# Optimization experiments

Hardware: AMD Instinct MI355X
Metric: run time of the kernel (lower is better)

The kernel has to match this reference:

```python
import jax, jax.numpy as jnp
import numpy as np
import math

B, C, H, W = 8, 256, 64, 64
CQK = C // 8

def _conv1x1(x, w, b):
    # x: [B,C,H,W], w: [O,C], b: [O]  (1x1 conv == per-pixel linear)
    return jnp.einsum('bchw,oc->bohw', x, w) + b[None, :, None, None]

def setup_inputs() -> dict:
    key = jax.random.key(0)
    ks = jax.random.split(key, 7)
    inputs = jax.random.normal(ks[0], (B, C, H, W), dtype=jnp.float32)
    # init_weight: normal(0, sqrt(2/(k*k*out_channels))) for 1x1 convs
    wq = jax.random.normal(ks[1], (CQK, C), dtype=jnp.float32) * math.sqrt(2.0 / CQK)
    wk = jax.random.normal(ks[2], (CQK, C), dtype=jnp.float32) * math.sqrt(2.0 / CQK)
    wv = jax.random.normal(ks[3], (C, C), dtype=jnp.float32) * math.sqrt(2.0 / C)
    bq = jnp.zeros((CQK,), dtype=jnp.float32)
    bk = jnp.zeros((CQK,), dtype=jnp.float32)
    bv = jnp.zeros((C,), dtype=jnp.float32)
    # torch init is zeros(1); use nonzero so the attention path contributes
    alpha = jnp.full((1,), 0.5, dtype=jnp.float32)
    return {"inputs": inputs, "wq": wq, "bq": bq, "wk": wk, "bk": bk,
            "wv": wv, "bv": bv, "alpha": alpha}

def reference(inputs, wq, bq, wk, bk, wv, bv, alpha):
    b, c, h, w = inputs.shape
    n = h * w
    q = _conv1x1(inputs, wq, bq).reshape(b, -1, n)          # [B, C/8, N]
    k = _conv1x1(inputs, wk, bk).reshape(b, -1, n)          # [B, C/8, N]
    v = _conv1x1(inputs, wv, bv).reshape(b, c, n)           # [B, C, N]
    # attention_weight[b, i, j] = q[:, i] . k[:, j]
    attn = jnp.einsum('bdi,bdj->bij', q, k)                 # [B, N, N]
    attn = jax.nn.softmax(attn, axis=-1)
    # value @ attn^T : out[b, c, i] = sum_j v[b, c, j] * attn[b, i, j]
    out = jnp.einsum('bcj,bij->bci', v, attn)               # [B, C, N]
    return alpha[0] * out.reshape(inputs.shape) + inputs
```

## Files before the change

### kernel.cpp

```cpp
#include <hip/hip_runtime.h>
#include <math.h>

#define B_  8
#define C_  256
#define N_  4096
#define NJC (N_ / 128)
#define PLD 136
#define LOG2E 1.4426950408889634f

using frag  = __attribute__((ext_vector_type(8))) short;
using f32x4 = __attribute__((ext_vector_type(4))) float;

__device__ __forceinline__ unsigned short f2bf(float f) {
    unsigned u = __float_as_uint(f);
    u += 0x7fffu + ((u >> 16) & 1u);
    return (unsigned short)(u >> 16);
}
__device__ __forceinline__ float bf2f(unsigned short h) {
    return __uint_as_float(((unsigned)h) << 16);
}
#define PK2(a, b) (((unsigned)(a)) | (((unsigned)(b)) << 16))

__device__ __forceinline__ f32x4 fmax4(f32x4 a, f32x4 b) {
    f32x4 r;
    r[0] = fmaxf(a[0], b[0]); r[1] = fmaxf(a[1], b[1]);
    r[2] = fmaxf(a[2], b[2]); r[3] = fmaxf(a[3], b[3]);
    return r;
}

__device__ __forceinline__ float exp2_raw(float x) {
    float r;
    asm("v_exp_f32 %0, %1" : "=v"(r) : "v"(x));
    return r;
}

__global__ __launch_bounds__(256) void wprep_kernel(
    const float* __restrict__ wq, const float* __restrict__ wk,
    const float* __restrict__ wv,
    unsigned short* __restrict__ whf, unsigned short* __restrict__ wlf)
{
    const int fid  = blockIdx.x * 256 + threadIdx.x;
    if (fid >= 20 * 8 * 64) return;
    const int g    = fid >> 9;
    const int kc   = (fid >> 6) & 7;
    const int lane = fid & 63;
    const int r16  = lane & 15, q = lane >> 4;

    const float* src; int row;
    if (g < 2)      { src = wq; row = g * 16 + r16; }
    else if (g < 4) { src = wk; row = (g - 2) * 16 + r16; }
    else            { src = wv; row = (g - 4) * 16 + r16; }

    const float scl = (g < 2) ? LOG2E : 1.0f;
    const float* wp = src + row * 256 + kc * 32 + q * 8;
    float v[8];
#pragma unroll
    for (int j = 0; j < 8; ++j) v[j] = wp[j] * scl;

    unsigned short h[8];
#pragma unroll
    for (int j = 0; j < 8; ++j) h[j] = f2bf(v[j]);
    uint4 U;
    U.x = PK2(h[0], h[1]); U.y = PK2(h[2], h[3]);
    U.z = PK2(h[4], h[5]); U.w = PK2(h[6], h[7]);
    *(uint4*)&whf[(size_t)fid * 8] = U;

    if (g < 4) {
        unsigned short l[8];
#pragma unroll
        for (int j = 0; j < 8; ++j) l[j] = f2bf(v[j] - bf2f(h[j]));
        uint4 V;
        V.x = PK2(l[0], l[1]); V.y = PK2(l[2], l[3]);
        V.z = PK2(l[4], l[5]); V.w = PK2(l[6], l[7]);
        *(uint4*)&wlf[(size_t)fid * 8] = V;
    }
}

__global__ __launch_bounds__(256, 4) void proj_kernel(
    const float* __restrict__ x,
    const float* __restrict__ bq, const float* __restrict__ bk,
    const float* __restrict__ bv,
    const unsigned short* __restrict__ whf, const unsigned short* __restrict__ wlf,
    unsigned short* __restrict__ qh, unsigned short* __restrict__ ql,
    unsigned short* __restrict__ kh, unsigned short* __restrict__ kl,
    unsigned short* __restrict__ vbf)
{
    __shared__ unsigned xpk[32 * 260 + 4];

    const int tid  = threadIdx.x;
    const int w    = tid >> 6;
    const int lane = tid & 63;
    const int quad = lane >> 4;
    const int l16  = lane & 15;
    const int n0   = blockIdx.x * 32;
    const int b    = blockIdx.y;

    {
        const int p  = tid & 31;
        const int cb = tid >> 5;
        const float* xbase = x + (size_t)b * C_ * N_ + n0 + p;
#pragma unroll 16
        for (int s = 0; s < 32; ++s) {
            const int c = s * 8 + cb;
            const float v = xbase[(size_t)c * N_];
            const unsigned short hb = f2bf(v);
            const unsigned short lb = f2bf(v - bf2f(hb));
            xpk[p * 260 + c] = (((unsigned)hb) << 16) | lb;
        }
    }
    __syncthreads();

    const frag* wh = (const frag*)whf;
    const frag* wl = (const frag*)wlf;

    f32x4 aqk[2];
    f32x4 av[4][2];
#pragma unroll
    for (int ps = 0; ps < 2; ++ps) {
        aqk[ps] = (f32x4){0.f, 0.f, 0.f, 0.f};
#pragma unroll
        for (int vg = 0; vg < 4; ++vg) av[vg][ps] = (f32x4){0.f, 0.f, 0.f, 0.f};
    }

    for (int kc = 0; kc < 8; ++kc) {
        const frag ah = wh[(w * 8 + kc) * 64 + lane];
        const frag al = wl[(w * 8 + kc) * 64 + lane];
        frag avw[4];
#pragma unroll
        for (int vg = 0; vg < 4; ++vg)
            avw[vg] = wh[((4 + w * 4 + vg) * 8 + kc) * 64 + lane];

#pragma unroll
        for (int ps = 0; ps < 2; ++ps) {
            const unsigned* row = &xpk[(ps * 16 + l16) * 260 + kc * 32 + quad * 8];
            const uint4 A  = *(const uint4*)row;
            const uint4 Bv = *(const uint4*)(row + 4);
            frag bh, bl;
            unsigned* bhp = (unsigned*)&bh;
            unsigned* blp = (unsigned*)&bl;
            bhp[0] = __builtin_amdgcn_perm(A.y,  A.x,  0x07060302u);
            bhp[1] = __builtin_amdgcn_perm(A.w,  A.z,  0x07060302u);
            bhp[2] = __builtin_amdgcn_perm(Bv.y, Bv.x, 0x07060302u);
            bhp[3] = __builtin_amdgcn_perm(Bv.w, Bv.z, 0x07060302u);
            blp[0] = __builtin_amdgcn_perm(A.y,  A.x,  0x05040100u);
            blp[1] = __builtin_amdgcn_perm(A.w,  A.z,  0x05040100u);
            blp[2] = __builtin_amdgcn_perm(Bv.y, Bv.x, 0x05040100u);
            blp[3] = __builtin_amdgcn_perm(Bv.w, Bv.z, 0x05040100u);

            aqk[ps] = __builtin_amdgcn_mfma_f32_16x16x32_bf16(ah, bh, aqk[ps], 0, 0, 0);
            aqk[ps] = __builtin_amdgcn_mfma_f32_16x16x32_bf16(al, bh, aqk[ps], 0, 0, 0);
            aqk[ps] = __builtin_amdgcn_mfma_f32_16x16x32_bf16(ah, bl, aqk[ps], 0, 0, 0);
#pragma unroll
            for (int vg = 0; vg < 4; ++vg)
                av[vg][ps] = __builtin_amdgcn_mfma_f32_16x16x32_bf16(
                    avw[vg], bh, av[vg][ps], 0, 0, 0);
        }
    }

    {
        const bool isq = (w < 2);
        const float* bias = isq ? bq : bk;
        const float bscl = isq ? LOG2E : 1.0f;
        const int dbase = (isq ? w : w - 2) * 16 + quad * 4;
        unsigned short* dsth = isq ? qh : kh;
        unsigned short* dstl = isq ? ql : kl;
        float bvals[4];
#pragma unroll
        for (int r = 0; r < 4; ++r) bvals[r] = bias[dbase + r] * bscl;
#pragma unroll
        for (int ps = 0; ps < 2; ++ps) {
            const int n = n0 + ps * 16 + l16;
            unsigned short hs[4], ls[4];
#pragma unroll
            for (int r = 0; r < 4; ++r) {
                const float f = aqk[ps][r] + bvals[r];
                hs[r] = f2bf(f);
                ls[r] = f2bf(f - bf2f(hs[r]));
            }
            const size_t off = ((size_t)(b * N_ + n)) * 32 + dbase;
            *(uint2*)&dsth[off] = make_uint2(PK2(hs[0], hs[1]), PK2(hs[2], hs[3]));
            *(uint2*)&dstl[off] = make_uint2(PK2(ls[0], ls[1]), PK2(ls[2], ls[3]));
        }
    }
#pragma unroll
    for (int vg = 0; vg < 4; ++vg)
#pragma unroll
        for (int ps = 0; ps < 2; ++ps) {
            const int n = n0 + ps * 16 + l16;
#pragma unroll
            for (int r = 0; r < 4; ++r) {
                const int c = (w * 4 + vg) * 16 + quad * 4 + r;
                vbf[((size_t)b * C_ + c) * N_ + n] = f2bf(av[vg][ps][r] + bv[c]);
            }
        }
}

__global__ __launch_bounds__(512, 2) void attn_kernel(
    const unsigned short* __restrict__ qh, const unsigned short* __restrict__ ql,
    const unsigned short* __restrict__ khg, const unsigned short* __restrict__ klg,
    const unsigned short* __restrict__ vbf,
    const float* __restrict__ x, const float* __restrict__ alpha_p,
    float* __restrict__ out)
{
    __shared__ __align__(16) short kbuf[2][2][128 * 32];
    __shared__ __align__(16) short p_s[2][128 * PLD];
    __shared__ __align__(16) float alpha_s[2][128];
    __shared__ __align__(16) float l_s[128];

    const int tid  = threadIdx.x;
    const int w    = tid >> 6;
    const int lane = tid & 63;
    const int quad = lane >> 4;
    const int l16  = lane & 15;
    const int bid  = blockIdx.x;
    const int b    = bid & 7;
    const int i0   = (bid >> 3) * 128;
    const int wi   = w >> 2;
    const int wc   = w & 3;

    const size_t qoff = ((size_t)(b * N_ + i0 + w * 16 + l16)) * 32 + quad * 8;
    const frag qhf = *(const frag*)(qh + qoff);
    const frag qlf = *(const frag*)(ql + qoff);

    const unsigned short* khb = khg + (size_t)b * N_ * 32;
    const unsigned short* klb = klg + (size_t)b * N_ * 32;
    const unsigned short* vb  = vbf + (size_t)b * C_ * N_;

    f32x4 o[4][4];
#pragma unroll
    for (int it = 0; it < 4; ++it)
#pragma unroll
        for (int ct = 0; ct < 4; ++ct)
            o[it][ct] = (f32x4){0.f, 0.f, 0.f, 0.f};

    float m_run = -INFINITY, l_run = 0.f;

    const int r_st  = w * 16 + l16;
    const int qc_st = quad;
    const int gsto  = r_st * 32 + qc_st * 8;
    const int lsto  = qc_st * 1024 + r_st * 8;

    frag vf[4][4];

    {
        const uint4 h0 = *(const uint4*)(khb + gsto);
        const uint4 l0 = *(const uint4*)(klb + gsto);
        *(uint4*)&kbuf[0][0][lsto] = h0;
        *(uint4*)&kbuf[0][1][lsto] = l0;
    }
    __syncthreads();

    for (int jc = 0; jc < NJC; ++jc) {
        const int bf = jc & 1;

        f32x4 st[8];
#pragma unroll
        for (int js = 0; js < 8; ++js) {
            const frag ka  = *(const frag*)&kbuf[bf][0][quad * 1024 + (js * 16 + l16) * 8];
            const frag kb2 = *(const frag*)&kbuf[bf][1][quad * 1024 + (js * 16 + l16) * 8];
            f32x4 s = (f32x4){0.f, 0.f, 0.f, 0.f};
            s = __builtin_amdgcn_mfma_f32_16x16x32_bf16(ka, qhf, s, 0, 0, 0);
            s = __builtin_amdgcn_mfma_f32_16x16x32_bf16(ka, qlf, s, 0, 0, 0);
            s = __builtin_amdgcn_mfma_f32_16x16x32_bf16(kb2, qhf, s, 0, 0, 0);
            st[js] = s;
        }

        const int jn = (jc + 1 < NJC) ? jc + 1 : jc;
        const uint4 knh = *(const uint4*)(khb + (size_t)jn * 4096 + gsto);
        const uint4 knl = *(const uint4*)(klb + (size_t)jn * 4096 + gsto);

        if (jc > 0) {
#pragma unroll
            for (int it = 0; it < 4; ++it) {
                const f32x4 alf = *(const f32x4*)&alpha_s[bf ^ 1][wi * 64 + it * 16 + quad * 4];
#pragma unroll
                for (int r = 0; r < 4; ++r) {
#pragma unroll
                    for (int ct = 0; ct < 4; ++ct) o[it][ct][r] *= alf[r];
                }
            }
#pragma unroll
            for (int ks = 0; ks < 4; ++ks) {
#pragma unroll
                for (int it = 0; it < 4; ++it) {
                    const frag pf = *(const frag*)&p_s[bf ^ 1][(wi * 64 + it * 16 + l16) * PLD
                                                              + ks * 32 + quad * 8];
#pragma unroll
                    for (int ct = 0; ct < 4; ++ct)
                        o[it][ct] = __builtin_amdgcn_mfma_f32_16x16x32_bf16(
                            pf, vf[ks][ct], o[it][ct], 0, 0, 0);
                }
            }
        }

#pragma unroll
        for (int ks = 0; ks < 4; ++ks)
#pragma unroll
            for (int ct = 0; ct < 4; ++ct)
                vf[ks][ct] = *(const frag*)(vb
                    + (size_t)(wc * 64 + ct * 16 + l16) * N_
                    + jc * 128 + ks * 32 + quad * 8);

        f32x4 t0 = fmax4(fmax4(st[0], st[1]), fmax4(st[2], st[3]));
        f32x4 t1 = fmax4(fmax4(st[4], st[5]), fmax4(st[6], st[7]));
        t0 = fmax4(t0, t1);
        float mx = fmaxf(fmaxf(t0[0], t0[1]), fmaxf(t0[2], t0[3]));
        mx = fmaxf(mx, __shfl_xor(mx, 16));
        mx = fmaxf(mx, __shfl_xor(mx, 32));
        const float mnew = fmaxf(m_run, mx);
        const float sc   = exp2_raw(m_run - mnew);

        f32x4 ps4 = (f32x4){0.f, 0.f, 0.f, 0.f};
#pragma unroll
        for (int js = 0; js < 8; ++js) {
#pragma unroll
            for (int r = 0; r < 4; ++r) st[js][r] = exp2_raw(st[js][r] - mnew);
            ps4[0] += st[js][0]; ps4[1] += st[js][1];
            ps4[2] += st[js][2]; ps4[3] += st[js][3];
        }
        float ps = (ps4[0] + ps4[1]) + (ps4[2] + ps4[3]);
        ps += __shfl_xor(ps, 16);
        ps += __shfl_xor(ps, 32);
        l_run = l_run * sc + ps;
        m_run = mnew;
        if (quad == 0) alpha_s[bf][w * 16 + l16] = sc;

#pragma unroll
        for (int js = 0; js < 8; ++js) {
            const unsigned a0 = __float_as_uint(st[js][0]) + 0x8000u;
            const unsigned a1 = __float_as_uint(st[js][1]) + 0x8000u;
            const unsigned a2 = __float_as_uint(st[js][2]) + 0x8000u;
            const unsigned a3 = __float_as_uint(st[js][3]) + 0x8000u;
            const unsigned p01 = __builtin_amdgcn_perm(a1, a0, 0x07060302u);
            const unsigned p23 = __builtin_amdgcn_perm(a3, a2, 0x07060302u);
            *(uint2*)&p_s[bf][(w * 16 + l16) * PLD + js * 16 + quad * 4] =
                make_uint2(p01, p23);
        }

        *(uint4*)&kbuf[bf ^ 1][0][lsto] = knh;
        *(uint4*)&kbuf[bf ^ 1][1][lsto] = knl;

        __syncthreads();
    }

    {
        const int bl = (NJC - 1) & 1;
#pragma unroll
        for (int it = 0; it < 4; ++it) {
            const f32x4 alf = *(const f32x4*)&alpha_s[bl][wi * 64 + it * 16 + quad * 4];
#pragma unroll
            for (int r = 0; r < 4; ++r) {
#pragma unroll
                for (int ct = 0; ct < 4; ++ct) o[it][ct][r] *= alf[r];
            }
        }
#pragma unroll
        for (int ks = 0; ks < 4; ++ks) {
#pragma unroll
            for (int it = 0; it < 4; ++it) {
                const frag pf = *(const frag*)&p_s[bl][(wi * 64 + it * 16 + l16) * PLD
                                                       + ks * 32 + quad * 8];
#pragma unroll
                for (int ct = 0; ct < 4; ++ct)
                    o[it][ct] = __builtin_amdgcn_mfma_f32_16x16x32_bf16(
                        pf, vf[ks][ct], o[it][ct], 0, 0, 0);
            }
        }
    }

    if (quad == 0) l_s[w * 16 + l16] = l_run;
    __syncthreads();
    const float av = alpha_p[0];

#pragma unroll
    for (int it = 0; it < 4; ++it) {
        const f32x4 lv = *(const f32x4*)&l_s[wi * 64 + it * 16 + quad * 4];
        float invl[4];
#pragma unroll
        for (int r = 0; r < 4; ++r) invl[r] = 1.f / lv[r];
#pragma unroll
        for (int ct = 0; ct < 4; ++ct) {
            const int c = wc * 64 + ct * 16 + l16;
            const size_t base = (size_t)b * C_ * N_ + (size_t)c * N_
                                + i0 + wi * 64 + it * 16 + quad * 4;
            const float4 xv = *(const float4*)(x + base);
            float4 ov;
            ov.x = av * (o[it][ct][0] * invl[0]) + xv.x;
            ov.y = av * (o[it][ct][1] * invl[1]) + xv.y;
            ov.z = av * (o[it][ct][2] * invl[2]) + xv.z;
            ov.w = av * (o[it][ct][3] * invl[3]) + xv.w;
            *(float4*)(out + base) = ov;
        }
    }
}

extern "C" void kernel_launch(void* const* d_in, const int* in_sizes, int n_in,
                              void* d_out, int out_size, void* d_ws, size_t ws_size,
                              hipStream_t stream)
{
    const float* x  = (const float*)d_in[0];
    const float* wq = (const float*)d_in[1];
    const float* bq = (const float*)d_in[2];
    const float* wk = (const float*)d_in[3];
    const float* bk = (const float*)d_in[4];
    const float* wv = (const float*)d_in[5];
    const float* bv = (const float*)d_in[6];
    const float* al = (const float*)d_in[7];
    float* out = (float*)d_out;

    char* ws = (char*)d_ws;
    unsigned short* qh  = (unsigned short*)(ws + 0);
    unsigned short* ql  = (unsigned short*)(ws + (size_t)2  * 1024 * 1024);
    unsigned short* kh  = (unsigned short*)(ws + (size_t)4  * 1024 * 1024);
    unsigned short* kl  = (unsigned short*)(ws + (size_t)6  * 1024 * 1024);
    unsigned short* vbf = (unsigned short*)(ws + (size_t)8  * 1024 * 1024);
    unsigned short* whf = (unsigned short*)(ws + (size_t)24 * 1024 * 1024);
    unsigned short* wlf = (unsigned short*)(ws + (size_t)24 * 1024 * 1024 + 256 * 1024);

    wprep_kernel<<<40, 256, 0, stream>>>(wq, wk, wv, whf, wlf);
    proj_kernel<<<dim3(N_ / 32, B_), 256, 0, stream>>>(
        x, bq, bk, bv, whf, wlf, qh, ql, kh, kl, vbf);
    attn_kernel<<<dim3(256), 512, 0, stream>>>(
        qh, ql, kh, kl, vbf, x, al, out);
}
```

Before: 252.0 us.

## Warp-specialize attention kernel into score/softmax and PV producer-consumer groups

Splits the 8 waves into two roles. Four waves compute QK scores and the online softmax for 32 rows each and write P to shared memory. The other four waves consume P from the previous chunk and accumulate the PV product over all 128 rows for their 64 channels. This aims to overlap the exp/softmax work with the MFMA-heavy PV stage through a one-chunk software pipeline. In exchange, each consumer wave holds twice as many accumulators (8x4 f32x4), which raises register pressure, and the producer waves sit idle during the epilogue.

```diff
diff --git a/kernel.cpp b/kernel.cpp
--- a/kernel.cpp
+++ b/kernel.cpp
@@ -215,32 +215,37 @@
     const int bid  = blockIdx.x;
     const int b    = bid & 7;
     const int i0   = (bid >> 3) * 128;
-    const int wi   = w >> 2;
-    const int wc   = w & 3;
-
-    const size_t qoff = ((size_t)(b * N_ + i0 + w * 16 + l16)) * 32 + quad * 8;
-    const frag qhf = *(const frag*)(qh + qoff);
-    const frag qlf = *(const frag*)(ql + qoff);
+    const bool isS = (w < 4);
+    const int  w2  = w & 3;
 
     const unsigned short* khb = khg + (size_t)b * N_ * 32;
     const unsigned short* klb = klg + (size_t)b * N_ * 32;
     const unsigned short* vb  = vbf + (size_t)b * C_ * N_;
 
-    f32x4 o[4][4];
-#pragma unroll
-    for (int it = 0; it < 4; ++it)
+    frag qhf[2], qlf[2];
+    if (isS) {
+#pragma unroll
+        for (int s2 = 0; s2 < 2; ++s2) {
+            const size_t qoff = ((size_t)(b * N_ + i0 + w2 * 32 + s2 * 16 + l16)) * 32
+                                + quad * 8;
+            qhf[s2] = *(const frag*)(qh + qoff);
+            qlf[s2] = *(const frag*)(ql + qoff);
+        }
+    }
+    float m_run[2] = {-INFINITY, -INFINITY};
+    float l_run[2] = {0.f, 0.f};
+
+    f32x4 o[8][4];
+#pragma unroll
+    for (int it = 0; it < 8; ++it)
 #pragma unroll
         for (int ct = 0; ct < 4; ++ct)
             o[it][ct] = (f32x4){0.f, 0.f, 0.f, 0.f};
-
-    float m_run = -INFINITY, l_run = 0.f;
 
     const int r_st  = w * 16 + l16;
     const int qc_st = quad;
     const int gsto  = r_st * 32 + qc_st * 8;
     const int lsto  = qc_st * 1024 + r_st * 8;
-
-    frag vf[4][4];
 
     {
         const uint4 h0 = *(const uint4*)(khb + gsto);
@@ -250,146 +255,146 @@
     }
     __syncthreads();
 
-    for (int jc = 0; jc < NJC; ++jc) {
-        const int bf = jc & 1;
-
-        f32x4 st[8];
-#pragma unroll
-        for (int js = 0; js < 8; ++js) {
-            const frag ka  = *(const frag*)&kbuf[bf][0][quad * 1024 + (js * 16 + l16) * 8];
-            const frag kb2 = *(const frag*)&kbuf[bf][1][quad * 1024 + (js * 16 + l16) * 8];
-            f32x4 s = (f32x4){0.f, 0.f, 0.f, 0.f};
-            s = __builtin_amdgcn_mfma_f32_16x16x32_bf16(ka, qhf, s, 0, 0, 0);
-            s = __builtin_amdgcn_mfma_f32_16x16x32_bf16(ka, qlf, s, 0, 0, 0);
-            s = __builtin_amdgcn_mfma_f32_16x16x32_bf16(kb2, qhf, s, 0, 0, 0);
-            st[js] = s;
-        }
-
-        const int jn = (jc + 1 < NJC) ? jc + 1 : jc;
-        const uint4 knh = *(const uint4*)(khb + (size_t)jn * 4096 + gsto);
-        const uint4 knl = *(const uint4*)(klb + (size_t)jn * 4096 + gsto);
-
-        if (jc > 0) {
-#pragma unroll
-            for (int it = 0; it < 4; ++it) {
-                const f32x4 alf = *(const f32x4*)&alpha_s[bf ^ 1][wi * 64 + it * 16 + quad * 4];
-#pragma unroll
-                for (int r = 0; r < 4; ++r) {
-#pragma unroll
-                    for (int ct = 0; ct < 4; ++ct) o[it][ct][r] *= alf[r];
+    for (int t = 0; t <= NJC; ++t) {
+        const int bf = t & 1;
+        const bool do_stage = (t + 1 < NJC);
+        uint4 knh, knl;
+        if (do_stage) {
+            knh = *(const uint4*)(khb + (size_t)(t + 1) * 4096 + gsto);
+            knl = *(const uint4*)(klb + (size_t)(t + 1) * 4096 + gsto);
+        }
+
+        if (isS) {
+            if (t < NJC) {
+                f32x4 st0[8], st1[8];
+#pragma unroll
+                for (int js = 0; js < 8; ++js) {
+                    const frag ka  = *(const frag*)&kbuf[bf][0][quad * 1024 + (js * 16 + l16) * 8];
+                    const frag kb2 = *(const frag*)&kbuf[bf][1][quad * 1024 + (js * 16 + l16) * 8];
+                    f32x4 s0 = (f32x4){0.f, 0.f, 0.f, 0.f};
+                    s0 = __builtin_amdgcn_mfma_f32_16x16x32_bf16(ka,  qhf[0], s0, 0, 0, 0);
+                    s0 = __builtin_amdgcn_mfma_f32_16x16x32_bf16(ka,  qlf[0], s0, 0, 0, 0);
+                    s0 = __builtin_amdgcn_mfma_f32_16x16x32_bf16(kb2, qhf[0], s0, 0, 0, 0);
+                    st0[js] = s0;
+                    f32x4 s1 = (f32x4){0.f, 0.f, 0.f, 0.f};
+                    s1 = __builtin_amdgcn_mfma_f32_16x16x32_bf16(ka,  qhf[1], s1, 0, 0, 0);
+                    s1 = __builtin_amdgcn_mfma_f32_16x16x32_bf16(ka,  qlf[1], s1, 0, 0, 0);
+                    s1 = __builtin_amdgcn_mfma_f32_16x16x32_bf16(kb2, qhf[1], s1, 0, 0, 0);
+                    st1[js] = s1;
+                }
+
+#pragma unroll
+                for (int s2 = 0; s2 < 2; ++s2) {
+                    f32x4* st = s2 ? st1 : st0;
+                    f32x4 t0v = fmax4(fmax4(st[0], st[1]), fmax4(st[2], st[3]));
+                    f32x4 t1v = fmax4(fmax4(st[4], st[5]), fmax4(st[6], st[7]));
+                    t0v = fmax4(t0v, t1v);
+                    float mx = fmaxf(fmaxf(t0v[0], t0v[1]), fmaxf(t0v[2], t0v[3]));
+                    mx = fmaxf(mx, __shfl_xor(mx, 16));
+                    mx = fmaxf(mx, __shfl_xor(mx, 32));
+                    const float mnew = fmaxf(m_run[s2], mx);
+                    const float sc   = exp2_raw(m_run[s2] - mnew);
+
+                    f32x4 ps4 = (f32x4){0.f, 0.f, 0.f, 0.f};
+#pragma unroll
+                    for (int js = 0; js < 8; ++js) {
+#pragma unroll
+                        for (int r = 0; r < 4; ++r) st[js][r] = exp2_raw(st[js][r] - mnew);
+                        ps4[0] += st[js][0]; ps4[1] += st[js][1];
+                        ps4[2] += st[js][2]; ps4[3] += st[js][3];
+                    }
+                    float ps = (ps4[0] + ps4[1]) + (ps4[2] + ps4[3]);
+                    ps += __shfl_xor(ps, 16);
+                    ps += __shfl_xor(ps, 32);
+                    l_run[s2] = l_run[s2] * sc + ps;
+                    m_run[s2] = mnew;
+                    const int row = w2 * 32 + s2 * 16 + l16;
+                    if (quad == 0) alpha_s[bf][row] = sc;
+
+#pragma unroll
+                    for (int js = 0; js < 8; ++js) {
+                        const unsigned a0 = __float_as_uint(st[js][0]) + 0x8000u;
+                        const unsigned a1 = __float_as_uint(st[js][1]) + 0x8000u;
+                        const unsigned a2 = __float_as_uint(st[js][2]) + 0x8000u;
+                        const unsigned a3 = __float_as_uint(st[js][3]) + 0x8000u;
+                        const unsigned p01 = __builtin_amdgcn_perm(a1, a0, 0x07060302u);
+                        const unsigned p23 = __builtin_amdgcn_perm(a3, a2, 0x07060302u);
+                        *(uint2*)&p_s[bf][row * PLD + js * 16 + quad * 4] =
+                            make_uint2(p01, p23);
+                    }
+                }
+            } else {
+                if (quad == 0) {
+                    l_s[w2 * 32 + l16]      = l_run[0];
+                    l_s[w2 * 32 + 16 + l16] = l_run[1];
                 }
             }
-#pragma unroll
-            for (int ks = 0; ks < 4; ++ks) {
-#pragma unroll
-                for (int it = 0; it < 4; ++it) {
-                    const frag pf = *(const frag*)&p_s[bf ^ 1][(wi * 64 + it * 16 + l16) * PLD
-                                                              + ks * 32 + quad * 8];
+        } else {
+            if (t > 0) {
+                const int pb = bf ^ 1;
+
+                frag vf[4][4];
+#pragma unroll
+                for (int ks = 0; ks < 4; ++ks)
 #pragma unroll
                     for (int ct = 0; ct < 4; ++ct)
-                        o[it][ct] = __builtin_amdgcn_mfma_f32_16x16x32_bf16(
-                            pf, vf[ks][ct], o[it][ct], 0, 0, 0);
+                        vf[ks][ct] = *(const frag*)(vb
+                            + (size_t)(w2 * 64 + ct * 16 + l16) * N_
+                            + (size_t)(t - 1) * 128 + ks * 32 + quad * 8);
+
+#pragma unroll
+                for (int it = 0; it < 8; ++it) {
+                    const f32x4 alf = *(const f32x4*)&alpha_s[pb][it * 16 + quad * 4];
+#pragma unroll
+                    for (int r = 0; r < 4; ++r) {
+#pragma unroll
+                        for (int ct = 0; ct < 4; ++ct) o[it][ct][r] *= alf[r];
+                    }
+                }
+
+#pragma unroll
+                for (int ks = 0; ks < 4; ++ks) {
+#pragma unroll
+                    for (int it = 0; it < 8; ++it) {
+                        const frag pf = *(const frag*)&p_s[pb][(it * 16 + l16) * PLD
+                                                               + ks * 32 + quad * 8];
+#pragma unroll
+                        for (int ct = 0; ct < 4; ++ct)
+                            o[it][ct] = __builtin_amdgcn_mfma_f32_16x16x32_bf16(
+                                pf, vf[ks][ct], o[it][ct], 0, 0, 0);
+                    }
                 }
             }
         }
 
-#pragma unroll
-        for (int ks = 0; ks < 4; ++ks)
-#pragma unroll
-            for (int ct = 0; ct < 4; ++ct)
-                vf[ks][ct] = *(const frag*)(vb
-                    + (size_t)(wc * 64 + ct * 16 + l16) * N_
-                    + jc * 128 + ks * 32 + quad * 8);
-
-        f32x4 t0 = fmax4(fmax4(st[0], st[1]), fmax4(st[2], st[3]));
-        f32x4 t1 = fmax4(fmax4(st[4], st[5]), fmax4(st[6], st[7]));
-        t0 = fmax4(t0, t1);
-        float mx = fmaxf(fmaxf(t0[0], t0[1]), fmaxf(t0[2], t0[3]));
-        mx = fmaxf(mx, __shfl_xor(mx, 16));
-        mx = fmaxf(mx, __shfl_xor(mx, 32));
-        const float mnew = fmaxf(m_run, mx);
-        const float sc   = exp2_raw(m_run - mnew);
-
-        f32x4 ps4 = (f32x4){0.f, 0.f, 0.f, 0.f};
-#pragma unroll
-        for (int js = 0; js < 8; ++js) {
-#pragma unroll
-            for (int r = 0; r < 4; ++r) st[js][r] = exp2_raw(st[js][r] - mnew);
-            ps4[0] += st[js][0]; ps4[1] += st[js][1];
-            ps4[2] += st[js][2]; ps4[3] += st[js][3];
-        }
-        float ps = (ps4[0] + ps4[1]) + (ps4[2] + ps4[3]);
-        ps += __shfl_xor(ps, 16);
-        ps += __shfl_xor(ps, 32);
-        l_run = l_run * sc + ps;
-        m_run = mnew;
-        if (quad == 0) alpha_s[bf][w * 16 + l16] = sc;
-
-#pragma unroll
-        for (int js = 0; js < 8; ++js) {
-            const unsigned a0 = __float_as_uint(st[js][0]) + 0x8000u;
-            const unsigned a1 = __float_as_uint(st[js][1]) + 0x8000u;
-            const unsigned a2 = __float_as_uint(st[js][2]) + 0x8000u;
-            const unsigned a3 = __float_as_uint(st[js][3]) + 0x8000u;
-            const unsigned p01 = __builtin_amdgcn_perm(a1, a0, 0x07060302u);
-            const unsigned p23 = __builtin_amdgcn_perm(a3, a2, 0x07060302u);
-            *(uint2*)&p_s[bf][(w * 16 + l16) * PLD + js * 16 + quad * 4] =
-                make_uint2(p01, p23);
-        }
-
-        *(uint4*)&kbuf[bf ^ 1][0][lsto] = knh;
-        *(uint4*)&kbuf[bf ^ 1][1][lsto] = knl;
-
+        if (do_stage) {
+            *(uint4*)&kbuf[bf ^ 1][0][lsto] = knh;
+            *(uint4*)&kbuf[bf ^ 1][1][lsto] = knl;
+        }
         __syncthreads();
     }
 
-    {
-        const int bl = (NJC - 1) & 1;
-#pragma unroll
-        for (int it = 0; it < 4; ++it) {
-            const f32x4 alf = *(const f32x4*)&alpha_s[bl][wi * 64 + it * 16 + quad * 4];
-#pragma unroll
-            for (int r = 0; r < 4; ++r) {
-#pragma unroll
-                for (int ct = 0; ct < 4; ++ct) o[it][ct][r] *= alf[r];
+    if (!isS) {
+        const float av = alpha_p[0];
+#pragma unroll
+        for (int it = 0; it < 8; ++it) {
+            const f32x4 lv = *(const f32x4*)&l_s[it * 16 + quad * 4];
+            float invl[4];
+#pragma unroll
+            for (int r = 0; r < 4; ++r) invl[r] = 1.f / lv[r];
+#pragma unroll
+            for (int ct = 0; ct < 4; ++ct) {
+                const int c = w2 * 64 + ct * 16 + l16;
+                const size_t base = (size_t)b * C_ * N_ + (size_t)c * N_
+                                    + i0 + it * 16 + quad * 4;
+                const float4 xv = *(const float4*)(x + base);
+                float4 ov;
+                ov.x = av * (o[it][ct][0] * invl[0]) + xv.x;
+                ov.y = av * (o[it][ct][1] * invl[1]) + xv.y;
+                ov.z = av * (o[it][ct][2] * invl[2]) + xv.z;
+                ov.w = av * (o[it][ct][3] * invl[3]) + xv.w;
+                *(float4*)(out + base) = ov;
             }
-        }
-#pragma unroll
-        for (int ks = 0; ks < 4; ++ks) {
-#pragma unroll
-            for (int it = 0; it < 4; ++it) {
-                const frag pf = *(const frag*)&p_s[bl][(wi * 64 + it * 16 + l16) * PLD
-                                                       + ks * 32 + quad * 8];
-#pragma unroll
-                for (int ct = 0; ct < 4; ++ct)
-                    o[it][ct] = __builtin_amdgcn_mfma_f32_16x16x32_bf16(
-                        pf, vf[ks][ct], o[it][ct], 0, 0, 0);
-            }
-        }
-    }
-
-    if (quad == 0) l_s[w * 16 + l16] = l_run;
-    __syncthreads();
-    const float av = alpha_p[0];
-
-#pragma unroll
-    for (int it = 0; it < 4; ++it) {
-        const f32x4 lv = *(const f32x4*)&l_s[wi * 64 + it * 16 + quad * 4];
-        float invl[4];
-#pragma unroll
-        for (int r = 0; r < 4; ++r) invl[r] = 1.f / lv[r];
-#pragma unroll
-        for (int ct = 0; ct < 4; ++ct) {
-            const int c = wc * 64 + ct * 16 + l16;
-            const size_t base = (size_t)b * C_ * N_ + (size_t)c * N_
-                                + i0 + wi * 64 + it * 16 + quad * 4;
-            const float4 xv = *(const float4*)(x + base);
-            float4 ov;
-            ov.x = av * (o[it][ct][0] * invl[0]) + xv.x;
-            ov.y = av * (o[it][ct][1] * invl[1]) + xv.y;
-            ov.z = av * (o[it][ct][2] * invl[2]) + xv.z;
-            ov.w = av * (o[it][ct][3] * invl[3]) + xv.w;
-            *(float4*)(out + base) = ov;
         }
     }
 }
```

After: 288.9 us. 1.15x slower.
